# Kernel optimization log

Measured on AMD Instinct MI355X. Metric: run time of the kernel, lower is better.

Reference implementation:

```python
import jax, jax.numpy as jnp
import numpy as np

# tanh-approximate GELU, matching F.gelu(..., approximate='tanh')
_SQRT_2_OVER_PI = 0.7978845608028654

def gelu_tanh(x):
    return 0.5 * x * (1.0 + jnp.tanh(_SQRT_2_OVER_PI * (x + 0.044715 * x * x * x)))

def setup_inputs() -> dict:
    key = jax.random.key(0)
    k1, k2, k3 = jax.random.split(key, 3)
    E, T, H, F = 8, 2048, 1024, 4096
    x = jax.random.normal(k1, (E, T, H), dtype=jnp.float32)
    w1 = jax.random.normal(k2, (E, H, F), dtype=jnp.float32) * (1.0 / np.sqrt(H))
    w2 = jax.random.normal(k3, (E, F, H), dtype=jnp.float32) * (1.0 / np.sqrt(F))
    return {"x": x, "w1": w1, "w2": w2}

def reference(x, w1, w2):
    # [E,T,H] @ [E,H,F] -> [E,T,F]
    h = jnp.einsum('eth,ehf->etf', x, w1)
    h = gelu_tanh(h)
    # [E,T,F] @ [E,F,H] -> [E,T,H]
    return jnp.einsum('etf,efh->eth', h, w2)
```

## Files before the change

### kernel.cpp

```cpp
#include <hip/hip_runtime.h>
#include <hip/hip_bf16.h>

typedef __attribute__((ext_vector_type(8))) short short8;
typedef __attribute__((ext_vector_type(4))) float f32x4;

typedef const __attribute__((address_space(1))) void* as1cv_t;
typedef __attribute__((address_space(3))) void* as3v_t;

__device__ __forceinline__ unsigned short f2bf(float f) {
    unsigned u = __float_as_uint(f);
    u += 0x7fffu + ((u >> 16) & 1u);
    return (unsigned short)(u >> 16);
}

__device__ __forceinline__ float gelu_tanh_f(float x) {
    float t = 0.7978845608028654f * (x + 0.044715f * x * x * x);
    float u = 2.0f * t;
    u = fminf(fmaxf(u, -30.0f), 30.0f);
    float e = __expf(u);
    float th = (e - 1.0f) / (e + 1.0f);
    return 0.5f * x * (1.0f + th);
}

__global__ void cvt_f32_to_bf16(const float* __restrict__ in,
                                unsigned short* __restrict__ out,
                                long long n) {
    long long i = (long long)blockIdx.x * blockDim.x + threadIdx.x;
    long long stride = (long long)gridDim.x * blockDim.x;
    const float4* in4 = (const float4*)in;
    ushort4* out4 = (ushort4*)out;
    long long n4 = n >> 2;
    for (long long j = i; j < n4; j += stride) {
        float4 v = in4[j];
        ushort4 o;
        o.x = f2bf(v.x); o.y = f2bf(v.y); o.z = f2bf(v.z); o.w = f2bf(v.w);
        out4[j] = o;
    }
}

__global__ void transpose_cvt(const float* __restrict__ in,
                              unsigned short* __restrict__ out,
                              int R, int C) {
    __shared__ float tile[32][33];
    int e = blockIdx.z;
    int c0 = blockIdx.x * 32;
    int r0 = blockIdx.y * 32;
    const float* ine = in + (size_t)e * R * C;
    unsigned short* oute = out + (size_t)e * R * C;
    int tx = threadIdx.x, ty = threadIdx.y;
#pragma unroll
    for (int i = 0; i < 4; i++) {
        tile[ty + i * 8][tx] = ine[(size_t)(r0 + ty + i * 8) * C + (c0 + tx)];
    }
    __syncthreads();
#pragma unroll
    for (int i = 0; i < 4; i++) {
        oute[(size_t)(c0 + ty + i * 8) * R + (r0 + tx)] = f2bf(tile[tx][ty + i * 8]);
    }
}

__device__ __forceinline__ void gload16(const void* g, void* l) {
    __builtin_amdgcn_global_load_lds((as1cv_t)g, (as3v_t)l, 16, 0, 0);
}

template <int DO_GELU>
__global__ __launch_bounds__(512, 2) void gemm256(
    const unsigned short* __restrict__ A,
    const unsigned short* __restrict__ Bt,
    void* __restrict__ Cout,
    int M, int N, int K, int tiles_m, int per_e, int nwg)
{
    int bid = blockIdx.x;
    int gbid = (bid & 7) * (nwg >> 3) + (bid >> 3);
    int e  = gbid / per_e;
    int t  = gbid % per_e;
    int bn = t / tiles_m;
    int bm = t % tiles_m;

    const unsigned short* Ae = A  + (size_t)e * M * K + (size_t)bm * 256 * K;
    const unsigned short* Be = Bt + (size_t)e * N * K + (size_t)bn * 256 * K;

    __shared__ alignas(16) unsigned short lds[3 * 16384];
    char* ldsc = (char*)lds;

    int tid  = threadIdx.x;
    int wid  = tid >> 6;
    int lane = tid & 63;
    int wave_m = wid >> 2;
    int wave_n = wid & 3;

    int c0 = wid * 64 + lane;
    int r0 = c0 >> 2;
    int r1 = r0 + 128;
    int kb = ((c0 & 3) << 4) ^ (((r0 >> 1) & 3) << 4);
    const char* gA0 = (const char*)(Ae + (size_t)r0 * K) + kb;
    const char* gA1 = (const char*)(Ae + (size_t)r1 * K) + kb;
    const char* gB0 = (const char*)(Be + (size_t)r0 * K) + kb;
    const char* gB1 = (const char*)(Be + (size_t)r1 * K) + kb;

    int xk = (((lane & 15) >> 1) & 3) << 4;
    int a_off = (wave_m * 128 + (lane & 15)) * 64 + ((((lane >> 4) << 4)) ^ xk);
    int b_off = 16384 + (wave_n * 64 + (lane & 15)) * 64 + ((((lane >> 4) << 4)) ^ xk);

    f32x4 acc[8][4];
    f32x4 zero = {0.0f, 0.0f, 0.0f, 0.0f};
#pragma unroll
    for (int i = 0; i < 8; i++)
#pragma unroll
        for (int j = 0; j < 4; j++) acc[i][j] = zero;

    unsigned bufC = 0, bufN = 32768, bufS = 65536;
    int NT = K >> 5;

#define STAGE(dst) do { \
        gload16(gA0, ldsc + (dst) + (wid << 10)); \
        gload16(gA1, ldsc + (dst) + 8192 + (wid << 10)); \
        gload16(gB0, ldsc + (dst) + 16384 + (wid << 10)); \
        gload16(gB1, ldsc + (dst) + 24576 + (wid << 10)); \
        gA0 += 64; gA1 += 64; gB0 += 64; gB1 += 64; } while (0)

    STAGE(bufC);
    STAGE(bufN);
    asm volatile("s_waitcnt vmcnt(4)" ::: "memory");
    __builtin_amdgcn_s_barrier();
    asm volatile("" ::: "memory");

    for (int kt = 0; kt < NT; ++kt) {
        bool more = (kt + 2) < NT;
        if (more) STAGE(bufS);

        const char* pa = ldsc + bufC + a_off;
        const char* pb = ldsc + bufC + b_off;

        short8 bf[4], af[4];
#pragma unroll
        for (int n = 0; n < 4; ++n) bf[n] = *(const short8*)(pb + n * 1024);
#pragma unroll
        for (int m = 0; m < 4; ++m) af[m] = *(const short8*)(pa + m * 1024);
        __builtin_amdgcn_s_setprio(1);
#pragma unroll
        for (int m = 0; m < 4; ++m)
#pragma unroll
            for (int n = 0; n < 4; ++n)
                acc[m][n] = __builtin_amdgcn_mfma_f32_16x16x32_bf16(af[m], bf[n], acc[m][n], 0, 0, 0);
        __builtin_amdgcn_s_setprio(0);

#pragma unroll
        for (int m = 0; m < 4; ++m) af[m] = *(const short8*)(pa + (m + 4) * 1024);
        __builtin_amdgcn_s_setprio(1);
#pragma unroll
        for (int m = 0; m < 4; ++m)
#pragma unroll
            for (int n = 0; n < 4; ++n)
                acc[m + 4][n] = __builtin_amdgcn_mfma_f32_16x16x32_bf16(af[m], bf[n], acc[m + 4][n], 0, 0, 0);
        __builtin_amdgcn_s_setprio(0);

        if (more) asm volatile("s_waitcnt vmcnt(4) lgkmcnt(0)" ::: "memory");
        else      asm volatile("s_waitcnt vmcnt(0) lgkmcnt(0)" ::: "memory");
        __builtin_amdgcn_sched_barrier(0);
        __builtin_amdgcn_s_barrier();
        asm volatile("" ::: "memory");

        unsigned tmp = bufC; bufC = bufN; bufN = bufS; bufS = tmp;
    }
#undef STAGE

    int row0 = bm * 256 + wave_m * 128 + ((lane >> 4) << 2);
    int col0 = bn * 256 + wave_n * 64 + (lane & 15);
    if (DO_GELU) {
        unsigned short* Ce = (unsigned short*)Cout + (size_t)e * M * N;
#pragma unroll
        for (int m = 0; m < 8; ++m)
#pragma unroll
            for (int n = 0; n < 4; ++n)
#pragma unroll
                for (int j = 0; j < 4; ++j) {
                    int row = row0 + m * 16 + j;
                    int col = col0 + n * 16;
                    Ce[(size_t)row * N + col] = f2bf(gelu_tanh_f(acc[m][n][j]));
                }
    } else {
        float* Ce = (float*)Cout + (size_t)e * M * N;
#pragma unroll
        for (int m = 0; m < 8; ++m)
#pragma unroll
            for (int n = 0; n < 4; ++n)
#pragma unroll
                for (int j = 0; j < 4; ++j) {
                    int row = row0 + m * 16 + j;
                    int col = col0 + n * 16;
                    Ce[(size_t)row * N + col] = acc[m][n][j];
                }
    }
}

extern "C" void kernel_launch(void* const* d_in, const int* in_sizes, int n_in,
                              void* d_out, int out_size, void* d_ws, size_t ws_size,
                              hipStream_t stream) {
    const float* x  = (const float*)d_in[0];
    const float* w1 = (const float*)d_in[1];
    const float* w2 = (const float*)d_in[2];
    float* out = (float*)d_out;

    const int E = 8, T = 2048, H = 1024, F = 4096;

    unsigned short* xb  = (unsigned short*)d_ws;
    unsigned short* w1t = xb  + (size_t)E * T * H;
    unsigned short* w2t = w1t + (size_t)E * H * F;
    unsigned short* hb  = w2t + (size_t)E * F * H;

    cvt_f32_to_bf16<<<2048, 256, 0, stream>>>(x, xb, (long long)E * T * H);

    dim3 tb(32, 8);
    transpose_cvt<<<dim3(F / 32, H / 32, E), tb, 0, stream>>>(w1, w1t, H, F);
    transpose_cvt<<<dim3(H / 32, F / 32, E), tb, 0, stream>>>(w2, w2t, F, H);

    {
        int M = T, N = F, K = H;
        int tiles_m = M / 256, per_e = tiles_m * (N / 256);
        int nwg = E * per_e;
        gemm256<1><<<nwg, 512, 0, stream>>>(xb, w1t, hb, M, N, K, tiles_m, per_e, nwg);
    }
    {
        int M = T, N = H, K = F;
        int tiles_m = M / 256, per_e = tiles_m * (N / 256);
        int nwg = E * per_e;
        gemm256<0><<<nwg, 512, 0, stream>>>(hb, w2t, out, M, N, K, tiles_m, per_e, nwg);
    }
}
```

Before: 414.9 us.

## Ping-pong GEMM main loop with 4-buffer LDS ring and split A/B staging; vectorize transpose

The GEMM main loop now uses a 4-slot LDS ring and splits each k-step into two halves. Global-to-LDS loads for A are issued in the first half and for B in the second, with barriers between the MFMA phases, so loads and matrix math interleave at a finer grain. This raises LDS use from 96KB to 128KB per block and adds more barriers per iteration, which may lower occupancy under launch_bounds(512,2). The weight transpose-convert kernel moves to 64x64 tiles with float4 loads and ushort4 stores to cut memory transactions.

```diff
diff --git a/kernel.cpp b/kernel.cpp
--- a/kernel.cpp
+++ b/kernel.cpp
@@ -38,24 +38,35 @@
     }
 }
 
-__global__ void transpose_cvt(const float* __restrict__ in,
-                              unsigned short* __restrict__ out,
-                              int R, int C) {
-    __shared__ float tile[32][33];
+__global__ void transpose_cvt64(const float* __restrict__ in,
+                                unsigned short* __restrict__ out,
+                                int R, int C) {
+    __shared__ float t[64][65];
     int e = blockIdx.z;
-    int c0 = blockIdx.x * 32;
-    int r0 = blockIdx.y * 32;
+    int c0 = blockIdx.x * 64;
+    int r0 = blockIdx.y * 64;
     const float* ine = in + (size_t)e * R * C;
     unsigned short* oute = out + (size_t)e * R * C;
-    int tx = threadIdx.x, ty = threadIdx.y;
+    int tid = threadIdx.x;
+    int lx = tid & 15, ly = tid >> 4;
 #pragma unroll
     for (int i = 0; i < 4; i++) {
-        tile[ty + i * 8][tx] = ine[(size_t)(r0 + ty + i * 8) * C + (c0 + tx)];
+        float4 v = *(const float4*)(ine + (size_t)(r0 + ly + i * 16) * C + c0 + lx * 4);
+        t[lx * 4 + 0][ly + i * 16] = v.x;
+        t[lx * 4 + 1][ly + i * 16] = v.y;
+        t[lx * 4 + 2][ly + i * 16] = v.z;
+        t[lx * 4 + 3][ly + i * 16] = v.w;
     }
     __syncthreads();
 #pragma unroll
     for (int i = 0; i < 4; i++) {
-        oute[(size_t)(c0 + ty + i * 8) * R + (r0 + tx)] = f2bf(tile[tx][ty + i * 8]);
+        int c = ly + i * 16;
+        ushort4 o;
+        o.x = f2bf(t[c][lx * 4 + 0]);
+        o.y = f2bf(t[c][lx * 4 + 1]);
+        o.z = f2bf(t[c][lx * 4 + 2]);
+        o.w = f2bf(t[c][lx * 4 + 3]);
+        *(ushort4*)(oute + (size_t)(c0 + c) * R + r0 + lx * 4) = o;
     }
 }
 
@@ -64,7 +75,7 @@
 }
 
 template <int DO_GELU>
-__global__ __launch_bounds__(512, 2) void gemm256(
+__global__ __launch_bounds__(512, 2) void gemm256p(
     const unsigned short* __restrict__ A,
     const unsigned short* __restrict__ Bt,
     void* __restrict__ Cout,
@@ -73,14 +84,14 @@
     int bid = blockIdx.x;
     int gbid = (bid & 7) * (nwg >> 3) + (bid >> 3);
     int e  = gbid / per_e;
-    int t  = gbid % per_e;
-    int bn = t / tiles_m;
-    int bm = t % tiles_m;
+    int t0_ = gbid % per_e;
+    int bn = t0_ / tiles_m;
+    int bm = t0_ % tiles_m;
 
     const unsigned short* Ae = A  + (size_t)e * M * K + (size_t)bm * 256 * K;
     const unsigned short* Be = Bt + (size_t)e * N * K + (size_t)bn * 256 * K;
 
-    __shared__ alignas(16) unsigned short lds[3 * 16384];
+    __shared__ alignas(16) unsigned short lds[4 * 16384];
     char* ldsc = (char*)lds;
 
     int tid  = threadIdx.x;
@@ -91,12 +102,12 @@
 
     int c0 = wid * 64 + lane;
     int r0 = c0 >> 2;
-    int r1 = r0 + 128;
     int kb = ((c0 & 3) << 4) ^ (((r0 >> 1) & 3) << 4);
     const char* gA0 = (const char*)(Ae + (size_t)r0 * K) + kb;
-    const char* gA1 = (const char*)(Ae + (size_t)r1 * K) + kb;
+    const char* gA1 = (const char*)(Ae + (size_t)(r0 + 128) * K) + kb;
     const char* gB0 = (const char*)(Be + (size_t)r0 * K) + kb;
-    const char* gB1 = (const char*)(Be + (size_t)r1 * K) + kb;
+    const char* gB1 = (const char*)(Be + (size_t)(r0 + 128) * K) + kb;
+    int sA = wid << 10;
 
     int xk = (((lane & 15) >> 1) & 3) << 4;
     int a_off = (wave_m * 128 + (lane & 15)) * 64 + ((((lane >> 4) << 4)) ^ xk);
@@ -109,34 +120,39 @@
 #pragma unroll
         for (int j = 0; j < 4; j++) acc[i][j] = zero;
 
-    unsigned bufC = 0, bufN = 32768, bufS = 65536;
     int NT = K >> 5;
 
-#define STAGE(dst) do { \
-        gload16(gA0, ldsc + (dst) + (wid << 10)); \
-        gload16(gA1, ldsc + (dst) + 8192 + (wid << 10)); \
-        gload16(gB0, ldsc + (dst) + 16384 + (wid << 10)); \
-        gload16(gB1, ldsc + (dst) + 24576 + (wid << 10)); \
-        gA0 += 64; gA1 += 64; gB0 += 64; gB1 += 64; } while (0)
-
-    STAGE(bufC);
-    STAGE(bufN);
+#define STAGE_A(dst) do { \
+        gload16(gA0, ldsc + (dst) + sA); \
+        gload16(gA1, ldsc + (dst) + 8192 + sA); \
+        gA0 += 64; gA1 += 64; } while (0)
+#define STAGE_B(dst) do { \
+        gload16(gB0, ldsc + (dst) + 16384 + sA); \
+        gload16(gB1, ldsc + (dst) + 24576 + sA); \
+        gB0 += 64; gB1 += 64; } while (0)
+
+    STAGE_A(0); STAGE_B(0);
+    STAGE_A(32768); STAGE_B(32768);
     asm volatile("s_waitcnt vmcnt(4)" ::: "memory");
     __builtin_amdgcn_s_barrier();
     asm volatile("" ::: "memory");
 
     for (int kt = 0; kt < NT; ++kt) {
+        unsigned bufT = (unsigned)(kt & 3) * 32768u;
+        unsigned bufS = (unsigned)((kt + 2) & 3) * 32768u;
         bool more = (kt + 2) < NT;
-        if (more) STAGE(bufS);
-
-        const char* pa = ldsc + bufC + a_off;
-        const char* pb = ldsc + bufC + b_off;
-
-        short8 bf[4], af[4];
+
+        const char* pa = ldsc + bufT + a_off;
+        const char* pb = ldsc + bufT + b_off;
+
+        short8 af[4], bf[4];
 #pragma unroll
         for (int n = 0; n < 4; ++n) bf[n] = *(const short8*)(pb + n * 1024);
 #pragma unroll
         for (int m = 0; m < 4; ++m) af[m] = *(const short8*)(pa + m * 1024);
+        if (more) STAGE_A(bufS);
+        __builtin_amdgcn_s_barrier();
+        asm volatile("s_waitcnt lgkmcnt(0)" ::: "memory");
         __builtin_amdgcn_s_setprio(1);
 #pragma unroll
         for (int m = 0; m < 4; ++m)
@@ -144,9 +160,15 @@
             for (int n = 0; n < 4; ++n)
                 acc[m][n] = __builtin_amdgcn_mfma_f32_16x16x32_bf16(af[m], bf[n], acc[m][n], 0, 0, 0);
         __builtin_amdgcn_s_setprio(0);
+        __builtin_amdgcn_s_barrier();
 
 #pragma unroll
         for (int m = 0; m < 4; ++m) af[m] = *(const short8*)(pa + (m + 4) * 1024);
+        if (more) STAGE_B(bufS);
+        if (more)              asm volatile("s_waitcnt vmcnt(4)" ::: "memory");
+        else if (kt + 1 < NT)  asm volatile("s_waitcnt vmcnt(0)" ::: "memory");
+        __builtin_amdgcn_s_barrier();
+        asm volatile("s_waitcnt lgkmcnt(0)" ::: "memory");
         __builtin_amdgcn_s_setprio(1);
 #pragma unroll
         for (int m = 0; m < 4; ++m)
@@ -154,16 +176,10 @@
             for (int n = 0; n < 4; ++n)
                 acc[m + 4][n] = __builtin_amdgcn_mfma_f32_16x16x32_bf16(af[m], bf[n], acc[m + 4][n], 0, 0, 0);
         __builtin_amdgcn_s_setprio(0);
-
-        if (more) asm volatile("s_waitcnt vmcnt(4) lgkmcnt(0)" ::: "memory");
-        else      asm volatile("s_waitcnt vmcnt(0) lgkmcnt(0)" ::: "memory");
-        __builtin_amdgcn_sched_barrier(0);
-        __builtin_amdgcn_s_barrier();
-        asm volatile("" ::: "memory");
-
-        unsigned tmp = bufC; bufC = bufN; bufN = bufS; bufS = tmp;
-    }
-#undef STAGE
+        __builtin_amdgcn_s_barrier();
+    }
+#undef STAGE_A
+#undef STAGE_B
 
     int row0 = bm * 256 + wave_m * 128 + ((lane >> 4) << 2);
     int col0 = bn * 256 + wave_n * 64 + (lane & 15);
@@ -211,20 +227,19 @@
 
     cvt_f32_to_bf16<<<2048, 256, 0, stream>>>(x, xb, (long long)E * T * H);
 
-    dim3 tb(32, 8);
-    transpose_cvt<<<dim3(F / 32, H / 32, E), tb, 0, stream>>>(w1, w1t, H, F);
-    transpose_cvt<<<dim3(H / 32, F / 32, E), tb, 0, stream>>>(w2, w2t, F, H);
+    transpose_cvt64<<<dim3(F / 64, H / 64, E), 256, 0, stream>>>(w1, w1t, H, F);
+    transpose_cvt64<<<dim3(H / 64, F / 64, E), 256, 0, stream>>>(w2, w2t, F, H);
 
     {
         int M = T, N = F, K = H;
         int tiles_m = M / 256, per_e = tiles_m * (N / 256);
         int nwg = E * per_e;
-        gemm256<1><<<nwg, 512, 0, stream>>>(xb, w1t, hb, M, N, K, tiles_m, per_e, nwg);
+        gemm256p<1><<<nwg, 512, 0, stream>>>(xb, w1t, hb, M, N, K, tiles_m, per_e, nwg);
     }
     {
         int M = T, N = H, K = F;
         int tiles_m = M / 256, per_e = tiles_m * (N / 256);
         int nwg = E * per_e;
-        gemm256<0><<<nwg, 512, 0, stream>>>(hb, w2t, out, M, N, K, tiles_m, per_e, nwg);
-    }
-}
+        gemm256p<0><<<nwg, 512, 0, stream>>>(hb, w2t, out, M, N, K, tiles_m, per_e, nwg);
+    }
+}
```

New measurement: 414.0 us. Within noise of the previous version (-0.2%).
